# Performance work log

Hardware: AMD Instinct MI355X
Metric: run time of the kernel (lower is better)

## Reference

```python
import jax, jax.numpy as jnp
import numpy as np

D = 32       # hidden_size (hardcoded in AR.__init__)
H = 16       # num_heads
HD = D // H  # head_dim = 2
L = 8        # num DiT blocks
MLP = 128    # mlp_ratio 4.0
B, S, T, P = 16, 1024, 256, 32
SCALE = float(1.0 / np.sqrt(HD))


def _ln(x, g, b, eps=1e-6):
    mu = jnp.mean(x, axis=-1, keepdims=True)
    var = jnp.mean((x - mu) ** 2, axis=-1, keepdims=True)
    return (x - mu) * jax.lax.rsqrt(var + eps) * g + b


def _mha(q_in, kv_in, in_w, in_b, out_w, out_b):
    # nn.MultiheadAttention math, batch-first layout (permutation-equivalent)
    wq, wk, wv = in_w[:D], in_w[D:2 * D], in_w[2 * D:]
    bq, bk, bv = in_b[:D], in_b[D:2 * D], in_b[2 * D:]
    Bq, Sq = q_in.shape[0], q_in.shape[1]
    Sk = kv_in.shape[1]
    q = (q_in @ wq.T + bq).reshape(Bq, Sq, H, HD)
    k = (kv_in @ wk.T + bk).reshape(Bq, Sk, H, HD)
    v = (kv_in @ wv.T + bv).reshape(Bq, Sk, H, HD)
    scores = jnp.einsum('bqhd,bkhd->bhqk', q, k) * SCALE
    a = jax.nn.softmax(scores, axis=-1)
    o = jnp.einsum('bhqk,bkhd->bqhd', a, v).reshape(Bq, Sq, D)
    return o @ out_w.T + out_b


def setup_inputs() -> dict:
    key = jax.random.key(0)
    ks = iter(jax.random.split(key, 40))
    rn = lambda k, sh, sc=1.0: jax.random.normal(k, sh, jnp.float32) * sc
    inp = {
        'x': rn(next(ks), (B, S, D)),
        'speaker_emb': rn(next(ks), (B, P, D)),
        'text_phonemes': rn(next(ks), (B, T, D)),
        'timestep_emb': rn(next(ks), (B, D)),
        'mask': jnp.ones((S,), jnp.float32),
        # per-block params, stacked over L for lax.scan
        'ln1_g': jnp.ones((L, D)), 'ln1_b': jnp.zeros((L, D)),
        'ln2_g': jnp.ones((L, D)), 'ln2_b': jnp.zeros((L, D)),
        'ln22_g': jnp.ones((L, D)), 'ln22_b': jnp.zeros((L, D)),
        'ln3_g': jnp.ones((L, D)), 'ln3_b': jnp.zeros((L, D)),
        'attn_in_w': rn(next(ks), (L, 3 * D, D), 0.1), 'attn_in_b': jnp.zeros((L, 3 * D)),
        'attn_out_w': rn(next(ks), (L, D, D), 0.1), 'attn_out_b': jnp.zeros((L, D)),
        'cross_in_w': rn(next(ks), (L, 3 * D, D), 0.1), 'cross_in_b': jnp.zeros((L, 3 * D)),
        'cross_out_w': rn(next(ks), (L, D, D), 0.1), 'cross_out_b': jnp.zeros((L, D)),
        'ts_w': rn(next(ks), (L, 2 * D, D), 0.1), 'ts_b': jnp.zeros((L, 2 * D)),
        'fc1_w': rn(next(ks), (L, MLP, D), 0.1), 'fc1_b': jnp.zeros((L, MLP)),
        'fc2_w': rn(next(ks), (L, D, MLP), 0.1), 'fc2_b': jnp.zeros((L, D)),
    }
    return inp


def _forward(x, speaker_emb, text_phonemes, timestep_emb, mask, params):
    m = mask[None, :, None]  # (1, S, 1), matches mask.unsqueeze(0).unsqueeze(2)
    def body(h, p):
        h = h * m
        hn = _ln(h, p['ln1_g'], p['ln1_b'])
        h = h + _mha(hn, hn, p['attn_in_w'], p['attn_in_b'], p['attn_out_w'], p['attn_out_b'])
        # both cross attentions use cross_attn weights (cross_attn2 is dead code in source)
        ca1 = _mha(_ln(h, p['ln2_g'], p['ln2_b']), text_phonemes,
                   p['cross_in_w'], p['cross_in_b'], p['cross_out_w'], p['cross_out_b'])
        ca2 = _mha(_ln(h, p['ln22_g'], p['ln22_b']), speaker_emb,
                   p['cross_in_w'], p['cross_in_b'], p['cross_out_w'], p['cross_out_b'])
        h = h + ca1 + ca2
        ss = timestep_emb @ p['ts_w'].T + p['ts_b']        # (B, 2D)
        scale, shift = ss[:, :D], ss[:, D:]
        hm = _ln(h, p['ln3_g'], p['ln3_b']) * (1.0 + scale[:, None, :]) + shift[:, None, :]
        mlp = jax.nn.gelu(hm @ p['fc1_w'].T + p['fc1_b'], approximate=False) @ p['fc2_w'].T + p['fc2_b']
        return (h + mlp) * m, None
    out, _ = jax.lax.scan(body, x, params)
    return out


def reference(x, speaker_emb, text_phonemes, timestep_emb, mask,
              ln1_g, ln1_b, ln2_g, ln2_b, ln22_g, ln22_b, ln3_g, ln3_b,
              attn_in_w, attn_in_b, attn_out_w, attn_out_b,
              cross_in_w, cross_in_b, cross_out_w, cross_out_b,
              ts_w, ts_b, fc1_w, fc1_b, fc2_w, fc2_b):
    params = dict(ln1_g=ln1_g, ln1_b=ln1_b, ln2_g=ln2_g, ln2_b=ln2_b,
                  ln22_g=ln22_g, ln22_b=ln22_b, ln3_g=ln3_g, ln3_b=ln3_b,
                  attn_in_w=attn_in_w, attn_in_b=attn_in_b,
                  attn_out_w=attn_out_w, attn_out_b=attn_out_b,
                  cross_in_w=cross_in_w, cross_in_b=cross_in_b,
                  cross_out_w=cross_out_w, cross_out_b=cross_out_b,
                  ts_w=ts_w, ts_b=ts_b, fc1_w=fc1_w, fc1_b=fc1_b,
                  fc2_w=fc2_w, fc2_b=fc2_b)
    return _forward(x, speaker_emb, text_phonemes, timestep_emb, mask, params)
```

## Files before the change

kernel.cpp:

```cpp
#include <hip/hip_runtime.h>
#include <math.h>

#define NB 16
#define SEQ 1024
#define NT 16384
#define TT 256
#define PP 32
#define NL 8
#define SCALE 0.70710678118654752f
#define LOG2E 1.4426950408889634f
#define CS (SCALE * LOG2E)

typedef float v2f __attribute__((ext_vector_type(2)));

static __device__ __forceinline__ float exp2fast(float x) {
#if __has_builtin(__builtin_amdgcn_exp2f)
  return __builtin_amdgcn_exp2f(x);
#else
  return exp2f(x);
#endif
}

__global__ __launch_bounds__(256) void k_pre(const float* __restrict__ tse,
                                             const float* __restrict__ tsw,
                                             const float* __restrict__ tsb,
                                             float* __restrict__ ssa,
                                             const float* __restrict__ text,
                                             const float* __restrict__ spk,
                                             const float* __restrict__ cw,
                                             const float* __restrict__ cb,
                                             float* __restrict__ kvtT,
                                             float* __restrict__ kvsT) {
  __shared__ float sh[64 * 33];
  int tid = threadIdx.x;
  int bx = blockIdx.x;
  if (bx < 32) {
    int idx = bx * 256 + tid;
    int l = idx >> 10;
    int rem = idx & 1023;
    int b = rem >> 6;
    int j = rem & 63;
    const float* wr = tsw + ((size_t)l * 64 + j) * 32;
    const float* xr = tse + b * 32;
    float acc = tsb[l * 64 + j];
#pragma unroll
    for (int e = 0; e < 32; e++) acc = fmaf(xr[e], wr[e], acc);
    ssa[idx] = acc;
    return;
  }
  const float* src;
  float* dst;
  int l, tok0, ntok;
  if (bx < 544) {
    l = (bx - 32) >> 6; tok0 = ((bx - 32) & 63) * 64; ntok = NB * TT; src = text;
    dst = kvtT + (size_t)l * 64 * ntok;
  } else {
    l = (bx - 544) >> 3; tok0 = ((bx - 544) & 7) * 64; ntok = NB * PP; src = spk;
    dst = kvsT + (size_t)l * 64 * ntok;
  }
  const float* w = cw + (size_t)l * 96 * 32 + 32 * 32;
  const float* wb = cb + (size_t)l * 96 + 32;
  for (int i = tid; i < 64 * 32; i += 256) {
    int tl = i >> 5, e = i & 31;
    sh[tl * 33 + e] = src[(size_t)(tok0 + tl) * 32 + e];
  }
  __syncthreads();
  int tl = tid & 63;
  int wv = tid >> 6;
#pragma unroll
  for (int k = 0; k < 16; k++) {
    int j = __builtin_amdgcn_readfirstlane(wv + 4 * k);
    const float* wr = w + j * 32;
    const float* hr = sh + tl * 33;
    float acc = wb[j];
#pragma unroll
    for (int e = 0; e < 32; e++) acc = fmaf(hr[e], wr[e], acc);
    dst[(size_t)j * ntok + tok0 + tl] = acc;
  }
}

__device__ __forceinline__ void load_row32(const float* __restrict__ base, int tok, float* r) {
#pragma unroll
  for (int e = 0; e < 32; e++) r[e] = base[(size_t)e * NT + tok];
}

__device__ __forceinline__ void ln_core(float* r) {
  float a0 = 0, a1 = 0, a2 = 0, a3 = 0;
#pragma unroll
  for (int e = 0; e < 32; e += 4) { a0 += r[e]; a1 += r[e + 1]; a2 += r[e + 2]; a3 += r[e + 3]; }
  float mu = ((a0 + a1) + (a2 + a3)) * (1.0f / 32.0f);
  float v0 = 0, v1 = 0, v2 = 0, v3 = 0;
#pragma unroll
  for (int e = 0; e < 32; e += 4) {
    float d0 = r[e] - mu, d1 = r[e + 1] - mu, d2 = r[e + 2] - mu, d3 = r[e + 3] - mu;
    v0 = fmaf(d0, d0, v0); v1 = fmaf(d1, d1, v1); v2 = fmaf(d2, d2, v2); v3 = fmaf(d3, d3, v3);
  }
  float rstd = rsqrtf(((v0 + v1) + (v2 + v3)) * (1.0f / 32.0f) + 1e-6f);
#pragma unroll
  for (int e = 0; e < 32; e++) r[e] = (r[e] - mu) * rstd;
}

__global__ __launch_bounds__(256) void k_qkv(const float* __restrict__ hin,
                                             int rowmajor,
                                             float* __restrict__ hT,
                                             const float* __restrict__ mask,
                                             const float* __restrict__ w,
                                             const float* __restrict__ wb,
                                             const float* __restrict__ g,
                                             const float* __restrict__ bv,
                                             float* __restrict__ qkvT) {
  int tid = threadIdx.x;
  int tok0 = blockIdx.x * 64;
  int yc = blockIdx.y;
  int tl = tid & 63, wv = tid >> 6;
  int tok = tok0 + tl;
  float r[32];
  if (rowmajor) {
    float m = mask[tok & (SEQ - 1)];
#pragma unroll
    for (int e = 0; e < 32; e++) r[e] = hin[(size_t)tok * 32 + e] * m;
    if (yc == 0 && wv == 0) {
#pragma unroll
      for (int e = 0; e < 32; e++) hT[(size_t)e * NT + tok] = r[e];
    }
  } else {
    load_row32(hin, tok, r);
  }
  ln_core(r);
#pragma unroll
  for (int e = 0; e < 32; e++) r[e] = fmaf(r[e], g[e], bv[e]);
#pragma unroll
  for (int k = 0; k < 6; k++) {
    int j = __builtin_amdgcn_readfirstlane(yc * 24 + wv + 4 * k);
    const float* wr = w + j * 32;
    float acc = wb[j];
#pragma unroll
    for (int e = 0; e < 32; e++) acc = fmaf(r[e], wr[e], acc);
    qkvT[(size_t)j * NT + tok] = acc;
  }
}

__global__ __launch_bounds__(256) void k_q12(const float* __restrict__ hT,
                                             const float* __restrict__ w,
                                             const float* __restrict__ wb,
                                             const float* __restrict__ g2, const float* __restrict__ b2,
                                             const float* __restrict__ g22, const float* __restrict__ b22,
                                             float* __restrict__ q1T, float* __restrict__ q2T) {
  int tid = threadIdx.x;
  int tok0 = blockIdx.x * 64, yc = blockIdx.y;
  int tl = tid & 63, wv = tid >> 6;
  int tok = tok0 + tl;
  float r[32];
  load_row32(hT, tok, r);
  ln_core(r);
  const float* g = (yc >= 2) ? g22 : g2;
  const float* bb = (yc >= 2) ? b22 : b2;
  float* dst = (yc >= 2) ? q2T : q1T;
#pragma unroll
  for (int e = 0; e < 32; e++) r[e] = fmaf(r[e], g[e], bb[e]);
  int jbase = (yc & 1) * 16;
#pragma unroll
  for (int k = 0; k < 4; k++) {
    int j = __builtin_amdgcn_readfirstlane(jbase + wv + 4 * k);
    const float* wr = w + j * 32;
    float acc = wb[j];
#pragma unroll
    for (int e = 0; e < 32; e++) acc = fmaf(r[e], wr[e], acc);
    dst[(size_t)j * NT + tok] = acc;
  }
}

__global__ __launch_bounds__(256) void k_proj_add(const float* __restrict__ s1T,
                                                  const float* __restrict__ s2T,
                                                  const float* __restrict__ w,
                                                  const float* __restrict__ wb, float bmult,
                                                  float* __restrict__ hT) {
  int tid = threadIdx.x;
  int tok0 = blockIdx.x * 64, yc = blockIdx.y;
  int tl = tid & 63, wv = tid >> 6;
  int tok = tok0 + tl;
  float r[32];
  if (s2T) {
#pragma unroll
    for (int e = 0; e < 32; e++)
      r[e] = s1T[(size_t)e * NT + tok] + s2T[(size_t)e * NT + tok];
  } else {
    load_row32(s1T, tok, r);
  }
#pragma unroll
  for (int k = 0; k < 2; k++) {
    int j = __builtin_amdgcn_readfirstlane(yc * 8 + wv + 4 * k);
    const float* wr = w + j * 32;
    float acc = bmult * wb[j];
#pragma unroll
    for (int e = 0; e < 32; e++) acc = fmaf(r[e], wr[e], acc);
    size_t gi = (size_t)j * NT + tok;
    hT[gi] += acc;
  }
}

template <int SK>
__device__ __forceinline__ void attn_core(const float* __restrict__ qb,
                                          const float* __restrict__ kb,
                                          const float* __restrict__ vb,
                                          int kvld,
                                          float* __restrict__ ob) {
  int tid = threadIdx.x;
  int bx = blockIdx.x;
  int rc = bx & 15, bh = bx >> 4;
  int b = bh >> 4, hh = bh & 15;
  int wv = tid >> 6, lane = tid & 63;
  int rg = lane >> 4, kl = lane & 15;
  int rbase = rc * 64 + wv * 16 + rg;

  const float* qx = qb + (size_t)(2 * hh) * NT + b * SEQ;
  const float* qy = qx + NT;
  const float* kx = kb + (size_t)(2 * hh) * kvld + b * SK;
  const float* ky = kx + kvld;
  const float* vx = vb + (size_t)(2 * hh) * kvld + b * SK;
  const float* vy = vx + kvld;

  v2f qxx[4], qyy[4], sum2[4], ox2[4], oy2[4];
#pragma unroll
  for (int s = 0; s < 4; s++) {
    float q1 = qx[rbase + 4 * s] * CS;
    float q2 = qy[rbase + 4 * s] * CS;
    qxx[s] = (v2f){q1, q1};
    qyy[s] = (v2f){q2, q2};
    sum2[s] = (v2f){0.f, 0.f};
    ox2[s] = (v2f){0.f, 0.f};
    oy2[s] = (v2f){0.f, 0.f};
  }

  if constexpr (SK >= 64) {
#pragma unroll 2
    for (int c = 0; c < SK / 64; c++) {
      int o = c * 64 + kl * 4;
      float4 kx4 = *(const float4*)(kx + o);
      float4 ky4 = *(const float4*)(ky + o);
      float4 vx4 = *(const float4*)(vx + o);
      float4 vy4 = *(const float4*)(vy + o);
      v2f kxlo = (v2f){kx4.x, kx4.y}, kxhi = (v2f){kx4.z, kx4.w};
      v2f kylo = (v2f){ky4.x, ky4.y}, kyhi = (v2f){ky4.z, ky4.w};
      v2f vxlo = (v2f){vx4.x, vx4.y}, vxhi = (v2f){vx4.z, vx4.w};
      v2f vylo = (v2f){vy4.x, vy4.y}, vyhi = (v2f){vy4.z, vy4.w};
#pragma unroll
      for (int s = 0; s < 4; s++) {
        v2f tlo = __builtin_elementwise_fma(qyy[s], kylo, qxx[s] * kxlo);
        v2f thi = __builtin_elementwise_fma(qyy[s], kyhi, qxx[s] * kxhi);
        v2f elo = (v2f){exp2fast(tlo[0]), exp2fast(tlo[1])};
        v2f ehi = (v2f){exp2fast(thi[0]), exp2fast(thi[1])};
        sum2[s] += elo;
        sum2[s] += ehi;
        ox2[s] = __builtin_elementwise_fma(elo, vxlo, ox2[s]);
        ox2[s] = __builtin_elementwise_fma(ehi, vxhi, ox2[s]);
        oy2[s] = __builtin_elementwise_fma(elo, vylo, oy2[s]);
        oy2[s] = __builtin_elementwise_fma(ehi, vyhi, oy2[s]);
      }
    }
  } else {
    v2f kx2 = *(const v2f*)(kx + kl * 2);
    v2f ky2 = *(const v2f*)(ky + kl * 2);
    v2f vx2 = *(const v2f*)(vx + kl * 2);
    v2f vy2 = *(const v2f*)(vy + kl * 2);
#pragma unroll
    for (int s = 0; s < 4; s++) {
      v2f t = __builtin_elementwise_fma(qyy[s], ky2, qxx[s] * kx2);
      v2f e = (v2f){exp2fast(t[0]), exp2fast(t[1])};
      sum2[s] += e;
      ox2[s] = __builtin_elementwise_fma(e, vx2, ox2[s]);
      oy2[s] = __builtin_elementwise_fma(e, vy2, oy2[s]);
    }
  }

#pragma unroll
  for (int s = 0; s < 4; s++) {
    float sm = sum2[s][0] + sum2[s][1];
    float ox = ox2[s][0] + ox2[s][1];
    float oy = oy2[s][0] + oy2[s][1];
#pragma unroll
    for (int off = 1; off < 16; off <<= 1) {
      sm += __shfl_xor(sm, off);
      ox += __shfl_xor(ox, off);
      oy += __shfl_xor(oy, off);
    }
    if (kl == 0) {
      float inv = 1.0f / sm;
      int tok = b * SEQ + rbase + 4 * s;
      ob[(size_t)(2 * hh) * NT + tok] = ox * inv;
      ob[(size_t)(2 * hh + 1) * NT + tok] = oy * inv;
    }
  }
}

__global__ __launch_bounds__(256) void k_attn_self(const float* __restrict__ qkvT,
                                                   float* __restrict__ oT) {
  attn_core<SEQ>(qkvT, qkvT + (size_t)32 * NT, qkvT + (size_t)64 * NT, NT, oT);
}

__global__ __launch_bounds__(256) void k_attn_cross(const float* __restrict__ q1T,
                                                    const float* __restrict__ q2T,
                                                    const float* __restrict__ kvt,
                                                    const float* __restrict__ kvs,
                                                    float* __restrict__ o1T,
                                                    float* __restrict__ o2T) {
  if (blockIdx.y == 0)
    attn_core<TT>(q1T, kvt, kvt + (size_t)32 * (NB * TT), NB * TT, o1T);
  else
    attn_core<PP>(q2T, kvs, kvs + (size_t)32 * (NB * PP), NB * PP, o2T);
}

__global__ __launch_bounds__(256) void k_fc1(const float* __restrict__ hT,
                                             const float* __restrict__ ssl,
                                             const float* __restrict__ g, const float* __restrict__ bv,
                                             const float* __restrict__ w1, const float* __restrict__ b1,
                                             float* __restrict__ uT) {
  int tid = threadIdx.x;
  int tok0 = blockIdx.x * 64, yc = blockIdx.y;
  int tl = tid & 63, wv = tid >> 6;
  int tok = tok0 + tl;
  int b = tok0 >> 10;
  const float* sc = ssl + b * 64;
  float r[32];
  load_row32(hT, tok, r);
  ln_core(r);
#pragma unroll
  for (int e = 0; e < 32; e++) {
    float ln = fmaf(r[e], g[e], bv[e]);
    r[e] = fmaf(ln, 1.0f + sc[e], sc[32 + e]);
  }
#pragma unroll
  for (int k = 0; k < 8; k++) {
    int j = __builtin_amdgcn_readfirstlane(yc * 32 + wv + 4 * k);
    const float* wr = w1 + j * 32;
    float acc = b1[j];
#pragma unroll
    for (int e = 0; e < 32; e++) acc = fmaf(r[e], wr[e], acc);
    float ge = 0.5f * acc * (1.0f + erff(acc * 0.70710678118654752f));
    uT[(size_t)j * NT + tok] = ge;
  }
}

__global__ __launch_bounds__(256) void k_fc2(const float* __restrict__ uT,
                                             float* __restrict__ hT,
                                             float* __restrict__ out_rm,
                                             const float* __restrict__ mask,
                                             const float* __restrict__ w2,
                                             const float* __restrict__ b2) {
  __shared__ __align__(16) float shu[64 * 132];
  int tid = threadIdx.x;
  int tok0 = blockIdx.x * 64, yc = blockIdx.y;
  for (int i = tid; i < 64 * 128; i += 256) {
    int e = i >> 6, tl = i & 63;
    shu[tl * 132 + e] = uT[(size_t)e * NT + tok0 + tl];
  }
  __syncthreads();
  int tl = tid & 63, wv = tid >> 6;
  int tok = tok0 + tl;
  int j0 = __builtin_amdgcn_readfirstlane(yc * 16 + wv);
  int j1 = __builtin_amdgcn_readfirstlane(j0 + 4);
  int j2 = __builtin_amdgcn_readfirstlane(j0 + 8);
  int j3 = __builtin_amdgcn_readfirstlane(j0 + 12);
  const float* w0 = w2 + j0 * 128;
  const float* w1 = w2 + j1 * 128;
  const float* w2r = w2 + j2 * 128;
  const float* w3 = w2 + j3 * 128;
  float a0 = b2[j0], a1 = b2[j1], a2 = b2[j2], a3 = b2[j3];
  const float4* ur = (const float4*)(shu + tl * 132);
#pragma unroll
  for (int m = 0; m < 32; m++) {
    float4 t = ur[m];
    a0 = fmaf(t.x, w0[4 * m], a0); a0 = fmaf(t.y, w0[4 * m + 1], a0);
    a0 = fmaf(t.z, w0[4 * m + 2], a0); a0 = fmaf(t.w, w0[4 * m + 3], a0);
    a1 = fmaf(t.x, w1[4 * m], a1); a1 = fmaf(t.y, w1[4 * m + 1], a1);
    a1 = fmaf(t.z, w1[4 * m + 2], a1); a1 = fmaf(t.w, w1[4 * m + 3], a1);
    a2 = fmaf(t.x, w2r[4 * m], a2); a2 = fmaf(t.y, w2r[4 * m + 1], a2);
    a2 = fmaf(t.z, w2r[4 * m + 2], a2); a2 = fmaf(t.w, w2r[4 * m + 3], a2);
    a3 = fmaf(t.x, w3[4 * m], a3); a3 = fmaf(t.y, w3[4 * m + 1], a3);
    a3 = fmaf(t.z, w3[4 * m + 2], a3); a3 = fmaf(t.w, w3[4 * m + 3], a3);
  }
  float mk = mask[tok & (SEQ - 1)];
  float r0 = (hT[(size_t)j0 * NT + tok] + a0) * mk;
  float r1 = (hT[(size_t)j1 * NT + tok] + a1) * mk;
  float r2 = (hT[(size_t)j2 * NT + tok] + a2) * mk;
  float r3 = (hT[(size_t)j3 * NT + tok] + a3) * mk;
  if (out_rm) {
    out_rm[(size_t)tok * 32 + j0] = r0;
    out_rm[(size_t)tok * 32 + j1] = r1;
    out_rm[(size_t)tok * 32 + j2] = r2;
    out_rm[(size_t)tok * 32 + j3] = r3;
  } else {
    hT[(size_t)j0 * NT + tok] = r0;
    hT[(size_t)j1 * NT + tok] = r1;
    hT[(size_t)j2 * NT + tok] = r2;
    hT[(size_t)j3 * NT + tok] = r3;
  }
}

extern "C" void kernel_launch(void* const* d_in, const int* in_sizes, int n_in,
                              void* d_out, int out_size, void* d_ws, size_t ws_size,
                              hipStream_t stream) {
  const float* x = (const float*)d_in[0];
  const float* spk = (const float*)d_in[1];
  const float* text = (const float*)d_in[2];
  const float* tse = (const float*)d_in[3];
  const float* mask = (const float*)d_in[4];
  const float* ln1_g = (const float*)d_in[5];
  const float* ln1_b = (const float*)d_in[6];
  const float* ln2_g = (const float*)d_in[7];
  const float* ln2_b = (const float*)d_in[8];
  const float* ln22_g = (const float*)d_in[9];
  const float* ln22_b = (const float*)d_in[10];
  const float* ln3_g = (const float*)d_in[11];
  const float* ln3_b = (const float*)d_in[12];
  const float* aw = (const float*)d_in[13];
  const float* ab = (const float*)d_in[14];
  const float* aow = (const float*)d_in[15];
  const float* aob = (const float*)d_in[16];
  const float* cw = (const float*)d_in[17];
  const float* cb = (const float*)d_in[18];
  const float* cow = (const float*)d_in[19];
  const float* cob = (const float*)d_in[20];
  const float* tsw = (const float*)d_in[21];
  const float* tsb = (const float*)d_in[22];
  const float* f1w = (const float*)d_in[23];
  const float* f1b = (const float*)d_in[24];
  const float* f2w = (const float*)d_in[25];
  const float* f2b = (const float*)d_in[26];

  float* ws = (float*)d_ws;
  float* hT = ws;
  float* qkvT = hT + (size_t)32 * NT;
  float* o1T = qkvT + (size_t)96 * NT;
  float* o2T = o1T + (size_t)32 * NT;
  float* q1T = o2T + (size_t)32 * NT;
  float* q2T = q1T + (size_t)32 * NT;
  float* kvtT = q2T + (size_t)32 * NT;
  float* kvsT = kvtT + (size_t)NL * 64 * (NB * TT);
  float* ssa = kvsT + (size_t)NL * 64 * (NB * PP);
  float* uT = o1T;

  k_pre<<<608, 256, 0, stream>>>(tse, tsw, tsb, ssa, text, spk, cw, cb, kvtT, kvsT);

  for (int l = 0; l < NL; l++) {
    k_qkv<<<dim3(256, 4), 256, 0, stream>>>((l == 0) ? x : hT, (l == 0) ? 1 : 0, hT, mask,
                                            aw + (size_t)l * 96 * 32, ab + l * 96,
                                            ln1_g + l * 32, ln1_b + l * 32, qkvT);
    k_attn_self<<<4096, 256, 0, stream>>>(qkvT, o1T);
    k_proj_add<<<dim3(256, 4), 256, 0, stream>>>(o1T, nullptr,
                                                 aow + (size_t)l * 32 * 32, aob + l * 32, 1.0f, hT);
    k_q12<<<dim3(256, 4), 256, 0, stream>>>(hT, cw + (size_t)l * 96 * 32, cb + l * 96,
                                            ln2_g + l * 32, ln2_b + l * 32,
                                            ln22_g + l * 32, ln22_b + l * 32, q1T, q2T);
    k_attn_cross<<<dim3(4096, 2), 256, 0, stream>>>(q1T, q2T,
                                                    kvtT + (size_t)l * 64 * (NB * TT),
                                                    kvsT + (size_t)l * 64 * (NB * PP),
                                                    o1T, o2T);
    k_proj_add<<<dim3(256, 4), 256, 0, stream>>>(o1T, o2T,
                                                 cow + (size_t)l * 32 * 32, cob + l * 32, 2.0f, hT);
    k_fc1<<<dim3(256, 4), 256, 0, stream>>>(hT, ssa + (size_t)l * NB * 64,
                                            ln3_g + l * 32, ln3_b + l * 32,
                                            f1w + (size_t)l * 128 * 32, f1b + l * 128, uT);
    k_fc2<<<dim3(256, 2), 256, 0, stream>>>(uT, hT, (l == NL - 1) ? (float*)d_out : nullptr,
                                            mask, f2w + (size_t)l * 32 * 128, f2b + l * 32);
  }
}
```

Baseline: 915.3 us.

## Fuse output projections with following LN+projection kernels, double attention rows per wave

Merges the self-attention output projection and residual add with the cross-attention query LN+projection, and the cross-attention output projection with the LN3+modulation+fc1 kernel. Residuals now ping-pong between two buffers instead of being updated in place. This cuts two launches per layer and several global round trips of the hidden state. Attention now processes 8 row sets per wave instead of 4, which halves the grid and increases K/V reuse. The cost is redundant projection work across the y-blocks of the fused kernels, fewer threads per kernel (64x2 and 64x4 blocks), and higher register pressure.

```diff
diff --git a/kernel.cpp b/kernel.cpp
--- a/kernel.cpp
+++ b/kernel.cpp
@@ -102,7 +102,7 @@
 
 __global__ __launch_bounds__(256) void k_qkv(const float* __restrict__ hin,
                                              int rowmajor,
-                                             float* __restrict__ hT,
+                                             float* __restrict__ hA,
                                              const float* __restrict__ mask,
                                              const float* __restrict__ w,
                                              const float* __restrict__ wb,
@@ -121,7 +121,7 @@
     for (int e = 0; e < 32; e++) r[e] = hin[(size_t)tok * 32 + e] * m;
     if (yc == 0 && wv == 0) {
 #pragma unroll
-      for (int e = 0; e < 32; e++) hT[(size_t)e * NT + tok] = r[e];
+      for (int e = 0; e < 32; e++) hA[(size_t)e * NT + tok] = r[e];
     }
   } else {
     load_row32(hin, tok, r);
@@ -140,78 +140,22 @@
   }
 }
 
-__global__ __launch_bounds__(256) void k_q12(const float* __restrict__ hT,
-                                             const float* __restrict__ w,
-                                             const float* __restrict__ wb,
-                                             const float* __restrict__ g2, const float* __restrict__ b2,
-                                             const float* __restrict__ g22, const float* __restrict__ b22,
-                                             float* __restrict__ q1T, float* __restrict__ q2T) {
-  int tid = threadIdx.x;
-  int tok0 = blockIdx.x * 64, yc = blockIdx.y;
-  int tl = tid & 63, wv = tid >> 6;
-  int tok = tok0 + tl;
-  float r[32];
-  load_row32(hT, tok, r);
-  ln_core(r);
-  const float* g = (yc >= 2) ? g22 : g2;
-  const float* bb = (yc >= 2) ? b22 : b2;
-  float* dst = (yc >= 2) ? q2T : q1T;
-#pragma unroll
-  for (int e = 0; e < 32; e++) r[e] = fmaf(r[e], g[e], bb[e]);
-  int jbase = (yc & 1) * 16;
-#pragma unroll
-  for (int k = 0; k < 4; k++) {
-    int j = __builtin_amdgcn_readfirstlane(jbase + wv + 4 * k);
-    const float* wr = w + j * 32;
-    float acc = wb[j];
-#pragma unroll
-    for (int e = 0; e < 32; e++) acc = fmaf(r[e], wr[e], acc);
-    dst[(size_t)j * NT + tok] = acc;
-  }
-}
-
-__global__ __launch_bounds__(256) void k_proj_add(const float* __restrict__ s1T,
-                                                  const float* __restrict__ s2T,
-                                                  const float* __restrict__ w,
-                                                  const float* __restrict__ wb, float bmult,
-                                                  float* __restrict__ hT) {
-  int tid = threadIdx.x;
-  int tok0 = blockIdx.x * 64, yc = blockIdx.y;
-  int tl = tid & 63, wv = tid >> 6;
-  int tok = tok0 + tl;
-  float r[32];
-  if (s2T) {
-#pragma unroll
-    for (int e = 0; e < 32; e++)
-      r[e] = s1T[(size_t)e * NT + tok] + s2T[(size_t)e * NT + tok];
-  } else {
-    load_row32(s1T, tok, r);
-  }
-#pragma unroll
-  for (int k = 0; k < 2; k++) {
-    int j = __builtin_amdgcn_readfirstlane(yc * 8 + wv + 4 * k);
-    const float* wr = w + j * 32;
-    float acc = bmult * wb[j];
-#pragma unroll
-    for (int e = 0; e < 32; e++) acc = fmaf(r[e], wr[e], acc);
-    size_t gi = (size_t)j * NT + tok;
-    hT[gi] += acc;
-  }
-}
-
-template <int SK>
+template <int SK, int SETS>
 __device__ __forceinline__ void attn_core(const float* __restrict__ qb,
                                           const float* __restrict__ kb,
                                           const float* __restrict__ vb,
                                           int kvld,
                                           float* __restrict__ ob) {
+  constexpr int RPW = 4 * SETS;
+  constexpr int RPB = 4 * RPW;
+  constexpr int NRC = SEQ / RPB;
   int tid = threadIdx.x;
   int bx = blockIdx.x;
-  int rc = bx & 15, bh = bx >> 4;
+  int rc = bx % NRC, bh = bx / NRC;
   int b = bh >> 4, hh = bh & 15;
   int wv = tid >> 6, lane = tid & 63;
   int rg = lane >> 4, kl = lane & 15;
-  int rbase = rc * 64 + wv * 16 + rg;
+  int rbase = rc * RPB + wv * RPW + rg;
 
   const float* qx = qb + (size_t)(2 * hh) * NT + b * SEQ;
   const float* qy = qx + NT;
@@ -220,9 +164,9 @@
   const float* vx = vb + (size_t)(2 * hh) * kvld + b * SK;
   const float* vy = vx + kvld;
 
-  v2f qxx[4], qyy[4], sum2[4], ox2[4], oy2[4];
-#pragma unroll
-  for (int s = 0; s < 4; s++) {
+  v2f qxx[SETS], qyy[SETS], sum2[SETS], ox2[SETS], oy2[SETS];
+#pragma unroll
+  for (int s = 0; s < SETS; s++) {
     float q1 = qx[rbase + 4 * s] * CS;
     float q2 = qy[rbase + 4 * s] * CS;
     qxx[s] = (v2f){q1, q1};
@@ -245,7 +189,7 @@
       v2f vxlo = (v2f){vx4.x, vx4.y}, vxhi = (v2f){vx4.z, vx4.w};
       v2f vylo = (v2f){vy4.x, vy4.y}, vyhi = (v2f){vy4.z, vy4.w};
 #pragma unroll
-      for (int s = 0; s < 4; s++) {
+      for (int s = 0; s < SETS; s++) {
         v2f tlo = __builtin_elementwise_fma(qyy[s], kylo, qxx[s] * kxlo);
         v2f thi = __builtin_elementwise_fma(qyy[s], kyhi, qxx[s] * kxhi);
         v2f elo = (v2f){exp2fast(tlo[0]), exp2fast(tlo[1])};
@@ -264,7 +208,7 @@
     v2f vx2 = *(const v2f*)(vx + kl * 2);
     v2f vy2 = *(const v2f*)(vy + kl * 2);
 #pragma unroll
-    for (int s = 0; s < 4; s++) {
+    for (int s = 0; s < SETS; s++) {
       v2f t = __builtin_elementwise_fma(qyy[s], ky2, qxx[s] * kx2);
       v2f e = (v2f){exp2fast(t[0]), exp2fast(t[1])};
       sum2[s] += e;
@@ -273,8 +217,10 @@
     }
   }
 
-#pragma unroll
-  for (int s = 0; s < 4; s++) {
+  float* oxr = ob + (size_t)(2 * hh) * NT + b * SEQ;
+  float* oyr = oxr + NT;
+#pragma unroll
+  for (int s = 0; s < SETS; s++) {
     float sm = sum2[s][0] + sum2[s][1];
     float ox = ox2[s][0] + ox2[s][1];
     float oy = oy2[s][0] + oy2[s][1];
@@ -286,16 +232,16 @@
     }
     if (kl == 0) {
       float inv = 1.0f / sm;
-      int tok = b * SEQ + rbase + 4 * s;
-      ob[(size_t)(2 * hh) * NT + tok] = ox * inv;
-      ob[(size_t)(2 * hh + 1) * NT + tok] = oy * inv;
+      int r = rbase + 4 * s;
+      oxr[r] = ox * inv;
+      oyr[r] = oy * inv;
     }
   }
 }
 
 __global__ __launch_bounds__(256) void k_attn_self(const float* __restrict__ qkvT,
                                                    float* __restrict__ oT) {
-  attn_core<SEQ>(qkvT, qkvT + (size_t)32 * NT, qkvT + (size_t)64 * NT, NT, oT);
+  attn_core<SEQ, 8>(qkvT, qkvT + (size_t)32 * NT, qkvT + (size_t)64 * NT, NT, oT);
 }
 
 __global__ __launch_bounds__(256) void k_attn_cross(const float* __restrict__ q1T,
@@ -305,44 +251,105 @@
                                                     float* __restrict__ o1T,
                                                     float* __restrict__ o2T) {
   if (blockIdx.y == 0)
-    attn_core<TT>(q1T, kvt, kvt + (size_t)32 * (NB * TT), NB * TT, o1T);
+    attn_core<TT, 8>(q1T, kvt, kvt + (size_t)32 * (NB * TT), NB * TT, o1T);
   else
-    attn_core<PP>(q2T, kvs, kvs + (size_t)32 * (NB * PP), NB * PP, o2T);
-}
-
-__global__ __launch_bounds__(256) void k_fc1(const float* __restrict__ hT,
-                                             const float* __restrict__ ssl,
-                                             const float* __restrict__ g, const float* __restrict__ bv,
-                                             const float* __restrict__ w1, const float* __restrict__ b1,
-                                             float* __restrict__ uT) {
-  int tid = threadIdx.x;
-  int tok0 = blockIdx.x * 64, yc = blockIdx.y;
-  int tl = tid & 63, wv = tid >> 6;
-  int tok = tok0 + tl;
-  int b = tok0 >> 10;
+    attn_core<PP, 8>(q2T, kvs, kvs + (size_t)32 * (NB * PP), NB * PP, o2T);
+}
+
+__global__ __launch_bounds__(256) void k_projq(const float* __restrict__ o1T,
+                                               const float* __restrict__ aow,
+                                               const float* __restrict__ aob,
+                                               const float* __restrict__ hA,
+                                               float* __restrict__ hB,
+                                               const float* __restrict__ cwq,
+                                               const float* __restrict__ cbq,
+                                               const float* __restrict__ g2, const float* __restrict__ b2,
+                                               const float* __restrict__ g22, const float* __restrict__ b22,
+                                               float* __restrict__ q1T, float* __restrict__ q2T) {
+  int tid = threadIdx.x;
+  int tok = blockIdx.x * 256 + tid;
+  int yc = blockIdx.y;
+  float o[32], h[32];
+  load_row32(o1T, tok, o);
+#pragma unroll
+  for (int e = 0; e < 32; e++) {
+    const float* wr = aow + e * 32;
+    float acc = aob[e];
+#pragma unroll
+    for (int i = 0; i < 32; i++) acc = fmaf(o[i], wr[i], acc);
+    h[e] = hA[(size_t)e * NT + tok] + acc;
+  }
+  if (yc == 0) {
+#pragma unroll
+    for (int e = 0; e < 32; e++) hB[(size_t)e * NT + tok] = h[e];
+  }
+  ln_core(h);
+  const float* g = yc ? g22 : g2;
+  const float* bb = yc ? b22 : b2;
+  float* dst = yc ? q2T : q1T;
+#pragma unroll
+  for (int e = 0; e < 32; e++) h[e] = fmaf(h[e], g[e], bb[e]);
+#pragma unroll
+  for (int j = 0; j < 32; j++) {
+    const float* wr = cwq + j * 32;
+    float acc = cbq[j];
+#pragma unroll
+    for (int i = 0; i < 32; i++) acc = fmaf(h[i], wr[i], acc);
+    dst[(size_t)j * NT + tok] = acc;
+  }
+}
+
+__global__ __launch_bounds__(256) void k_proj_fc1(const float* __restrict__ o1T,
+                                                  const float* __restrict__ o2T,
+                                                  const float* __restrict__ cow,
+                                                  const float* __restrict__ cob,
+                                                  const float* __restrict__ hB,
+                                                  float* __restrict__ hC,
+                                                  const float* __restrict__ ssl,
+                                                  const float* __restrict__ g, const float* __restrict__ bv,
+                                                  const float* __restrict__ w1, const float* __restrict__ b1,
+                                                  float* __restrict__ uT) {
+  int tid = threadIdx.x;
+  int tok = blockIdx.x * 256 + tid;
+  int yc = blockIdx.y;
+  int b = tok >> 10;
+  float o[32], h[32];
+#pragma unroll
+  for (int e = 0; e < 32; e++)
+    o[e] = o1T[(size_t)e * NT + tok] + o2T[(size_t)e * NT + tok];
+#pragma unroll
+  for (int e = 0; e < 32; e++) {
+    const float* wr = cow + e * 32;
+    float acc = 2.0f * cob[e];
+#pragma unroll
+    for (int i = 0; i < 32; i++) acc = fmaf(o[i], wr[i], acc);
+    h[e] = hB[(size_t)e * NT + tok] + acc;
+  }
+  if (yc == 0) {
+#pragma unroll
+    for (int e = 0; e < 32; e++) hC[(size_t)e * NT + tok] = h[e];
+  }
+  ln_core(h);
   const float* sc = ssl + b * 64;
-  float r[32];
-  load_row32(hT, tok, r);
-  ln_core(r);
 #pragma unroll
   for (int e = 0; e < 32; e++) {
-    float ln = fmaf(r[e], g[e], bv[e]);
-    r[e] = fmaf(ln, 1.0f + sc[e], sc[32 + e]);
-  }
-#pragma unroll
-  for (int k = 0; k < 8; k++) {
-    int j = __builtin_amdgcn_readfirstlane(yc * 32 + wv + 4 * k);
+    float ln = fmaf(h[e], g[e], bv[e]);
+    h[e] = fmaf(ln, 1.0f + sc[e], sc[32 + e]);
+  }
+#pragma unroll
+  for (int k = 0; k < 32; k++) {
+    int j = yc * 32 + k;
     const float* wr = w1 + j * 32;
     float acc = b1[j];
 #pragma unroll
-    for (int e = 0; e < 32; e++) acc = fmaf(r[e], wr[e], acc);
+    for (int i = 0; i < 32; i++) acc = fmaf(h[i], wr[i], acc);
     float ge = 0.5f * acc * (1.0f + erff(acc * 0.70710678118654752f));
     uT[(size_t)j * NT + tok] = ge;
   }
 }
 
 __global__ __launch_bounds__(256) void k_fc2(const float* __restrict__ uT,
-                                             float* __restrict__ hT,
+                                             float* hio,
                                              float* __restrict__ out_rm,
                                              const float* __restrict__ mask,
                                              const float* __restrict__ w2,
@@ -380,20 +387,22 @@
     a3 = fmaf(t.z, w3[4 * m + 2], a3); a3 = fmaf(t.w, w3[4 * m + 3], a3);
   }
   float mk = mask[tok & (SEQ - 1)];
-  float r0 = (hT[(size_t)j0 * NT + tok] + a0) * mk;
-  float r1 = (hT[(size_t)j1 * NT + tok] + a1) * mk;
-  float r2 = (hT[(size_t)j2 * NT + tok] + a2) * mk;
-  float r3 = (hT[(size_t)j3 * NT + tok] + a3) * mk;
+  size_t g0 = (size_t)j0 * NT + tok, g1 = (size_t)j1 * NT + tok;
+  size_t g2i = (size_t)j2 * NT + tok, g3 = (size_t)j3 * NT + tok;
+  float r0 = (hio[g0] + a0) * mk;
+  float r1 = (hio[g1] + a1) * mk;
+  float r2 = (hio[g2i] + a2) * mk;
+  float r3 = (hio[g3] + a3) * mk;
   if (out_rm) {
     out_rm[(size_t)tok * 32 + j0] = r0;
     out_rm[(size_t)tok * 32 + j1] = r1;
     out_rm[(size_t)tok * 32 + j2] = r2;
     out_rm[(size_t)tok * 32 + j3] = r3;
   } else {
-    hT[(size_t)j0 * NT + tok] = r0;
-    hT[(size_t)j1 * NT + tok] = r1;
-    hT[(size_t)j2 * NT + tok] = r2;
-    hT[(size_t)j3 * NT + tok] = r3;
+    hio[g0] = r0;
+    hio[g1] = r1;
+    hio[g2i] = r2;
+    hio[g3] = r3;
   }
 }
 
@@ -429,39 +438,41 @@
   const float* f2b = (const float*)d_in[26];
 
   float* ws = (float*)d_ws;
-  float* hT = ws;
-  float* qkvT = hT + (size_t)32 * NT;
-  float* o1T = qkvT + (size_t)96 * NT;
-  float* o2T = o1T + (size_t)32 * NT;
-  float* q1T = o2T + (size_t)32 * NT;
-  float* q2T = q1T + (size_t)32 * NT;
-  float* kvtT = q2T + (size_t)32 * NT;
+  const size_t SL = (size_t)32 * NT;
+  float* uT = ws;
+  float* qkvT = ws;
+  float* q1T = ws;
+  float* q2T = ws + SL;
+  float* hA = ws + 4 * SL;
+  float* o1T = ws + 5 * SL;
+  float* o2T = ws + 6 * SL;
+  float* hB = ws + 7 * SL;
+  float* kvtT = ws + 8 * SL;
   float* kvsT = kvtT + (size_t)NL * 64 * (NB * TT);
   float* ssa = kvsT + (size_t)NL * 64 * (NB * PP);
-  float* uT = o1T;
 
   k_pre<<<608, 256, 0, stream>>>(tse, tsw, tsb, ssa, text, spk, cw, cb, kvtT, kvsT);
 
   for (int l = 0; l < NL; l++) {
-    k_qkv<<<dim3(256, 4), 256, 0, stream>>>((l == 0) ? x : hT, (l == 0) ? 1 : 0, hT, mask,
+    k_qkv<<<dim3(256, 4), 256, 0, stream>>>((l == 0) ? x : hA, (l == 0) ? 1 : 0, hA, mask,
                                             aw + (size_t)l * 96 * 32, ab + l * 96,
                                             ln1_g + l * 32, ln1_b + l * 32, qkvT);
-    k_attn_self<<<4096, 256, 0, stream>>>(qkvT, o1T);
-    k_proj_add<<<dim3(256, 4), 256, 0, stream>>>(o1T, nullptr,
-                                                 aow + (size_t)l * 32 * 32, aob + l * 32, 1.0f, hT);
-    k_q12<<<dim3(256, 4), 256, 0, stream>>>(hT, cw + (size_t)l * 96 * 32, cb + l * 96,
-                                            ln2_g + l * 32, ln2_b + l * 32,
-                                            ln22_g + l * 32, ln22_b + l * 32, q1T, q2T);
-    k_attn_cross<<<dim3(4096, 2), 256, 0, stream>>>(q1T, q2T,
+    k_attn_self<<<2048, 256, 0, stream>>>(qkvT, o1T);
+    k_projq<<<dim3(64, 2), 256, 0, stream>>>(o1T, aow + (size_t)l * 32 * 32, aob + l * 32,
+                                             hA, hB,
+                                             cw + (size_t)l * 96 * 32, cb + l * 96,
+                                             ln2_g + l * 32, ln2_b + l * 32,
+                                             ln22_g + l * 32, ln22_b + l * 32, q1T, q2T);
+    k_attn_cross<<<dim3(2048, 2), 256, 0, stream>>>(q1T, q2T,
                                                     kvtT + (size_t)l * 64 * (NB * TT),
                                                     kvsT + (size_t)l * 64 * (NB * PP),
                                                     o1T, o2T);
-    k_proj_add<<<dim3(256, 4), 256, 0, stream>>>(o1T, o2T,
-                                                 cow + (size_t)l * 32 * 32, cob + l * 32, 2.0f, hT);
-    k_fc1<<<dim3(256, 4), 256, 0, stream>>>(hT, ssa + (size_t)l * NB * 64,
-                                            ln3_g + l * 32, ln3_b + l * 32,
-                                            f1w + (size_t)l * 128 * 32, f1b + l * 128, uT);
-    k_fc2<<<dim3(256, 2), 256, 0, stream>>>(uT, hT, (l == NL - 1) ? (float*)d_out : nullptr,
+    k_proj_fc1<<<dim3(64, 4), 256, 0, stream>>>(o1T, o2T,
+                                                cow + (size_t)l * 32 * 32, cob + l * 32,
+                                                hB, hA, ssa + (size_t)l * NB * 64,
+                                                ln3_g + l * 32, ln3_b + l * 32,
+                                                f1w + (size_t)l * 128 * 32, f1b + l * 128, uT);
+    k_fc2<<<dim3(256, 2), 256, 0, stream>>>(uT, hA, (l == NL - 1) ? (float*)d_out : nullptr,
                                             mask, f2w + (size_t)l * 32 * 128, f2b + l * 32);
   }
 }
```

Result: slower. 1.311 ms (+43.2%).

## Stage token rows in LDS and share LayerNorm across waves in projection kernels

Applied to the files above, without the earlier changes.

The QKV, cross-query and projection-add kernels now load each 64-token tile once into padded shared memory. The LayerNorm for each token is computed once by the first wave and stored in shared memory, instead of every wave redoing it in registers. The later dot products read their inputs from LDS. This cuts redundant global loads and duplicated LayerNorm work, and makes the row-major input load coalesced. In exchange it adds two block barriers, leaves three waves idle during the LayerNorm, replaces register operands with LDS reads, and now has every y-block write the transposed hidden state and apply the mask in both paths.

```diff
diff --git a/kernel.cpp b/kernel.cpp
--- a/kernel.cpp
+++ b/kernel.cpp
@@ -109,34 +109,53 @@
                                              const float* __restrict__ g,
                                              const float* __restrict__ bv,
                                              float* __restrict__ qkvT) {
+  __shared__ float shr[64 * 33];
+  __shared__ float shn[64 * 33];
   int tid = threadIdx.x;
   int tok0 = blockIdx.x * 64;
   int yc = blockIdx.y;
+  if (rowmajor) {
+    for (int i = tid; i < 2048; i += 256) {
+      int tl = i >> 5, e = i & 31;
+      float m = mask[(tok0 + tl) & (SEQ - 1)];
+      shr[tl * 33 + e] = hin[(size_t)(tok0 + tl) * 32 + e] * m;
+    }
+  } else {
+    for (int i = tid; i < 2048; i += 256) {
+      int e = i >> 6, tl = i & 63;
+      float m = mask[(tok0 + tl) & (SEQ - 1)];
+      shr[tl * 33 + e] = hin[(size_t)e * NT + tok0 + tl] * m;
+    }
+  }
+  __syncthreads();
+  for (int i = tid; i < 2048; i += 256) {
+    int e = i >> 6, tl = i & 63;
+    hT[(size_t)e * NT + tok0 + tl] = shr[tl * 33 + e];
+  }
+  if (tid < 64) {
+    float mu = 0.f;
+#pragma unroll
+    for (int e = 0; e < 32; e++) mu += shr[tid * 33 + e];
+    mu *= (1.0f / 32.0f);
+    float var = 0.f;
+#pragma unroll
+    for (int e = 0; e < 32; e++) { float d = shr[tid * 33 + e] - mu; var = fmaf(d, d, var); }
+    float rstd = rsqrtf(var * (1.0f / 32.0f) + 1e-6f);
+#pragma unroll
+    for (int e = 0; e < 32; e++)
+      shn[tid * 33 + e] = (shr[tid * 33 + e] - mu) * rstd * g[e] + bv[e];
+  }
+  __syncthreads();
   int tl = tid & 63, wv = tid >> 6;
-  int tok = tok0 + tl;
-  float r[32];
-  if (rowmajor) {
-    float m = mask[tok & (SEQ - 1)];
-#pragma unroll
-    for (int e = 0; e < 32; e++) r[e] = hin[(size_t)tok * 32 + e] * m;
-    if (yc == 0 && wv == 0) {
-#pragma unroll
-      for (int e = 0; e < 32; e++) hT[(size_t)e * NT + tok] = r[e];
-    }
-  } else {
-    load_row32(hin, tok, r);
-  }
-  ln_core(r);
-#pragma unroll
-  for (int e = 0; e < 32; e++) r[e] = fmaf(r[e], g[e], bv[e]);
 #pragma unroll
   for (int k = 0; k < 6; k++) {
     int j = __builtin_amdgcn_readfirstlane(yc * 24 + wv + 4 * k);
     const float* wr = w + j * 32;
+    const float* hr = shn + tl * 33;
     float acc = wb[j];
 #pragma unroll
-    for (int e = 0; e < 32; e++) acc = fmaf(r[e], wr[e], acc);
-    qkvT[(size_t)j * NT + tok] = acc;
+    for (int e = 0; e < 32; e++) acc = fmaf(hr[e], wr[e], acc);
+    qkvT[(size_t)j * NT + tok0 + tl] = acc;
   }
 }
 
@@ -146,27 +165,46 @@
                                              const float* __restrict__ g2, const float* __restrict__ b2,
                                              const float* __restrict__ g22, const float* __restrict__ b22,
                                              float* __restrict__ q1T, float* __restrict__ q2T) {
-  int tid = threadIdx.x;
-  int tok0 = blockIdx.x * 64, yc = blockIdx.y;
+  __shared__ float shr[64 * 33];
+  __shared__ float shn[2][64 * 33];
+  int tid = threadIdx.x;
+  int tok0 = blockIdx.x * 64;
+  int yc = blockIdx.y;
+  for (int i = tid; i < 2048; i += 256) {
+    int e = i >> 6, tl = i & 63;
+    shr[tl * 33 + e] = hT[(size_t)e * NT + tok0 + tl];
+  }
+  __syncthreads();
+  if (tid < 64) {
+    float mu = 0.f;
+#pragma unroll
+    for (int e = 0; e < 32; e++) mu += shr[tid * 33 + e];
+    mu *= (1.0f / 32.0f);
+    float var = 0.f;
+#pragma unroll
+    for (int e = 0; e < 32; e++) { float d = shr[tid * 33 + e] - mu; var = fmaf(d, d, var); }
+    float rstd = rsqrtf(var * (1.0f / 32.0f) + 1e-6f);
+#pragma unroll
+    for (int e = 0; e < 32; e++) {
+      float core = (shr[tid * 33 + e] - mu) * rstd;
+      shn[0][tid * 33 + e] = core * g2[e] + b2[e];
+      shn[1][tid * 33 + e] = core * g22[e] + b22[e];
+    }
+  }
+  __syncthreads();
   int tl = tid & 63, wv = tid >> 6;
-  int tok = tok0 + tl;
-  float r[32];
-  load_row32(hT, tok, r);
-  ln_core(r);
-  const float* g = (yc >= 2) ? g22 : g2;
-  const float* bb = (yc >= 2) ? b22 : b2;
-  float* dst = (yc >= 2) ? q2T : q1T;
-#pragma unroll
-  for (int e = 0; e < 32; e++) r[e] = fmaf(r[e], g[e], bb[e]);
-  int jbase = (yc & 1) * 16;
 #pragma unroll
   for (int k = 0; k < 4; k++) {
-    int j = __builtin_amdgcn_readfirstlane(jbase + wv + 4 * k);
+    int jj = __builtin_amdgcn_readfirstlane(yc * 16 + wv + 4 * k);
+    int which = jj >> 5;
+    int j = jj & 31;
     const float* wr = w + j * 32;
+    const float* hr = shn[which] + tl * 33;
     float acc = wb[j];
 #pragma unroll
-    for (int e = 0; e < 32; e++) acc = fmaf(r[e], wr[e], acc);
-    dst[(size_t)j * NT + tok] = acc;
+    for (int e = 0; e < 32; e++) acc = fmaf(hr[e], wr[e], acc);
+    float* dst = which ? q2T : q1T;
+    dst[(size_t)j * NT + tok0 + tl] = acc;
   }
 }
 
@@ -175,26 +213,27 @@
                                                   const float* __restrict__ w,
                                                   const float* __restrict__ wb, float bmult,
                                                   float* __restrict__ hT) {
-  int tid = threadIdx.x;
-  int tok0 = blockIdx.x * 64, yc = blockIdx.y;
+  __shared__ float sh[64 * 33];
+  int tid = threadIdx.x;
+  int tok0 = blockIdx.x * 64;
+  int yc = blockIdx.y;
+  for (int i = tid; i < 2048; i += 256) {
+    int e = i >> 6, tl = i & 63;
+    float v = s1T[(size_t)e * NT + tok0 + tl];
+    if (s2T) v += s2T[(size_t)e * NT + tok0 + tl];
+    sh[tl * 33 + e] = v;
+  }
+  __syncthreads();
   int tl = tid & 63, wv = tid >> 6;
-  int tok = tok0 + tl;
-  float r[32];
-  if (s2T) {
-#pragma unroll
-    for (int e = 0; e < 32; e++)
-      r[e] = s1T[(size_t)e * NT + tok] + s2T[(size_t)e * NT + tok];
-  } else {
-    load_row32(s1T, tok, r);
-  }
 #pragma unroll
   for (int k = 0; k < 2; k++) {
     int j = __builtin_amdgcn_readfirstlane(yc * 8 + wv + 4 * k);
     const float* wr = w + j * 32;
+    const float* hr = sh + tl * 33;
     float acc = bmult * wb[j];
 #pragma unroll
-    for (int e = 0; e < 32; e++) acc = fmaf(r[e], wr[e], acc);
-    size_t gi = (size_t)j * NT + tok;
+    for (int e = 0; e < 32; e++) acc = fmaf(hr[e], wr[e], acc);
+    size_t gi = (size_t)j * NT + tok0 + tl;
     hT[gi] += acc;
   }
 }
@@ -342,7 +381,7 @@
 }
 
 __global__ __launch_bounds__(256) void k_fc2(const float* __restrict__ uT,
-                                             float* __restrict__ hT,
+                                             float* hT,
                                              float* __restrict__ out_rm,
                                              const float* __restrict__ mask,
                                              const float* __restrict__ w2,
@@ -380,20 +419,22 @@
     a3 = fmaf(t.z, w3[4 * m + 2], a3); a3 = fmaf(t.w, w3[4 * m + 3], a3);
   }
   float mk = mask[tok & (SEQ - 1)];
-  float r0 = (hT[(size_t)j0 * NT + tok] + a0) * mk;
-  float r1 = (hT[(size_t)j1 * NT + tok] + a1) * mk;
-  float r2 = (hT[(size_t)j2 * NT + tok] + a2) * mk;
-  float r3 = (hT[(size_t)j3 * NT + tok] + a3) * mk;
+  size_t g0 = (size_t)j0 * NT + tok, g1 = (size_t)j1 * NT + tok;
+  size_t g2i = (size_t)j2 * NT + tok, g3 = (size_t)j3 * NT + tok;
+  float r0 = (hT[g0] + a0) * mk;
+  float r1 = (hT[g1] + a1) * mk;
+  float r2 = (hT[g2i] + a2) * mk;
+  float r3 = (hT[g3] + a3) * mk;
   if (out_rm) {
     out_rm[(size_t)tok * 32 + j0] = r0;
     out_rm[(size_t)tok * 32 + j1] = r1;
     out_rm[(size_t)tok * 32 + j2] = r2;
     out_rm[(size_t)tok * 32 + j3] = r3;
   } else {
-    hT[(size_t)j0 * NT + tok] = r0;
-    hT[(size_t)j1 * NT + tok] = r1;
-    hT[(size_t)j2 * NT + tok] = r2;
-    hT[(size_t)j3 * NT + tok] = r3;
+    hT[g0] = r0;
+    hT[g1] = r1;
+    hT[g2i] = r2;
+    hT[g3] = r3;
   }
 }
 
```

Measured after the change: 1.014 ms. +10.8%, slower.
